# Optimization experiments

Measured on AMD Instinct MI355X. Metric: run time of the kernel, lower is better.

The kernel has to match this reference:

```python
import jax, jax.numpy as jnp
import numpy as np

B, C, H, W = 4, 512, 64, 64
CQ = C // 8  # query/key channels = 64


def setup_inputs() -> dict:
    key = jax.random.key(0)
    ks = jax.random.split(key, 6)
    return {
        "x_spatial": jax.random.normal(ks[0], (B, C, H, W), jnp.float32),
        "x_temporal": jax.random.normal(ks[1], (B, C, H, W), jnp.float32),
        "Wq": jax.random.normal(ks[2], (CQ, C), jnp.float32) * (1.0 / np.sqrt(C)),
        "bq": jnp.zeros((CQ,), jnp.float32),
        "Wk": jax.random.normal(ks[3], (CQ, C), jnp.float32) * (1.0 / np.sqrt(C)),
        "bk": jnp.zeros((CQ,), jnp.float32),
        "Wvs": jax.random.normal(ks[4], (C, C), jnp.float32) * (1.0 / np.sqrt(C)),
        "bvs": jnp.zeros((C,), jnp.float32),
        "Wvt": jax.random.normal(ks[5], (C, C), jnp.float32) * (1.0 / np.sqrt(C)),
        "bvt": jnp.zeros((C,), jnp.float32),
    }


def reference(x_spatial, x_temporal, Wq, bq, Wk, bk, Wvs, bvs, Wvt, bvt):
    b, c, h, w = x_spatial.shape
    n = h * w
    xs = x_spatial.reshape(b, c, n)   # (B, C, N)
    xt = x_temporal.reshape(b, c, n)
    # 1x1 convs == pointwise linear over channels
    q = jnp.einsum('qc,bcn->bnq', Wq, xs) + bq            # (B, N, CQ)
    k = jnp.einsum('qc,bcn->bqn', Wk, xt) + bk[:, None]    # (B, CQ, N)
    scale = (c // 8) ** -0.5
    energy = scale * jnp.einsum('bnq,bqm->bnm', q, k)      # (B, N, N)
    attn = jax.nn.softmax(energy, axis=-1)
    v_s = jnp.einsum('oc,bcn->bon', Wvs, xs) + bvs[:, None]  # (B, C, N)
    v_t = jnp.einsum('oc,bcn->bon', Wvt, xt) + bvt[:, None]
    # out[b,c,i] = sum_j v[b,c,j] * attn[b,i,j]
    out1 = jnp.einsum('bcj,bij->bci', v_s, attn)
    out2 = jnp.einsum('bcj,bij->bci', v_t, attn)
    out = out1.reshape(b, c, h, w) + x_spatial + out2.reshape(b, c, h, w) + x_temporal
    return out
```

## Files before the change

### kernel.cpp

```cpp
#include <hip/hip_runtime.h>
#include <hip/hip_bf16.h>
#include <math.h>

#define NTOK 4096
#define CH 512
#define CQD 64
#define NBATCH 4
#define JB 128

typedef __bf16 bf16x8 __attribute__((ext_vector_type(8)));
typedef float f32x4 __attribute__((ext_vector_type(4)));
typedef unsigned int u32x4 __attribute__((ext_vector_type(4)));
typedef unsigned short u16x4 __attribute__((ext_vector_type(4)));

__device__ __forceinline__ unsigned short f2bf(float f) {
  unsigned int u = __builtin_bit_cast(unsigned int, f);
  unsigned int r = (u + 0x7FFFu + ((u >> 16) & 1u)) >> 16;
  return (unsigned short)r;
}

__device__ __forceinline__ bf16x8 load_frag(const unsigned short* p) {
  u32x4 v = *reinterpret_cast<const u32x4*>(p);
  return __builtin_bit_cast(bf16x8, v);
}

__global__ void k_transpose(const float* __restrict__ xs, const float* __restrict__ xt,
                            unsigned short* __restrict__ xT) {
  __shared__ unsigned short lds[64][66];
  int b = blockIdx.z;
  int n0 = blockIdx.x * 64;
  int c0 = blockIdx.y * 64;
  const float* src = (c0 < CH) ? xs : xt;
  int cs0 = (c0 < CH) ? c0 : c0 - CH;
  int tid = threadIdx.x;
  int nn = tid & 63, cg = tid >> 6;
  const float* base = src + ((size_t)b * CH + cs0) * NTOK + n0;
  for (int cc = cg; cc < 64; cc += 4)
    lds[cc][nn] = f2bf(base[(size_t)cc * NTOK + nn]);
  __syncthreads();
  int cw = tid & 63, ng = tid >> 6;
  unsigned short* dst = xT + ((size_t)b * NTOK + n0) * 1024 + c0 + cw;
  for (int n2 = ng; n2 < 64; n2 += 4)
    dst[(size_t)n2 * 1024] = lds[cw][n2];
}

__global__ void k_weights(const float* __restrict__ Wq, const float* __restrict__ Wk,
                          const float* __restrict__ Wvs, const float* __restrict__ Wvt,
                          unsigned short* __restrict__ wq, unsigned short* __restrict__ wk,
                          unsigned short* __restrict__ wv) {
  int t = blockIdx.x * 256 + threadIdx.x;
  if (t < 32768) {
    wq[t] = f2bf(Wq[t]);
  } else if (t < 65536) {
    int j = t - 32768;
    wk[j] = f2bf(Wk[j]);
  } else {
    int j = t - 65536;
    if (j < 512 * 1024) {
      int c = j >> 10, k = j & 1023;
      float v = (k < 512) ? Wvs[c * 512 + k] : Wvt[c * 512 + (k - 512)];
      wv[j] = f2bf(v);
    }
  }
}

__global__ void __launch_bounds__(256)
k_proj(const unsigned short* __restrict__ xT, const unsigned short* __restrict__ W,
       const float* __restrict__ bias1, const float* __restrict__ bias2,
       unsigned short* __restrict__ out, int Kdim, int koff, int mode) {
  int b = blockIdx.z;
  int n0 = blockIdx.x * 256;
  int m0 = blockIdx.y * 64;
  int tid = threadIdx.x;
  int w = tid >> 6, l = tid & 63;
  int fr = l & 15, fk = l >> 4;
  f32x4 acc[4][4] = {};
  const unsigned short* xbase =
      xT + ((size_t)b * NTOK + n0 + w * 64 + fr) * 1024 + koff + fk * 8;
  const unsigned short* wbase = W + ((size_t)(m0 + fr)) * Kdim + fk * 8;
  for (int k = 0; k < Kdim; k += 32) {
    bf16x8 a[4], bb[4];
#pragma unroll
    for (int ns = 0; ns < 4; ns++) a[ns] = load_frag(xbase + (size_t)ns * 16 * 1024 + k);
#pragma unroll
    for (int mf = 0; mf < 4; mf++) bb[mf] = load_frag(wbase + (size_t)mf * 16 * Kdim + k);
#pragma unroll
    for (int ns = 0; ns < 4; ns++)
#pragma unroll
      for (int mf = 0; mf < 4; mf++)
        acc[ns][mf] = __builtin_amdgcn_mfma_f32_16x16x32_bf16(a[ns], bb[mf], acc[ns][mf], 0, 0, 0);
  }
  if (mode == 0) {
#pragma unroll
    for (int ns = 0; ns < 4; ns++)
#pragma unroll
      for (int mf = 0; mf < 4; mf++) {
        int m = m0 + mf * 16 + fr;
        float bv = bias1[m];
        int nb = n0 + w * 64 + ns * 16 + fk * 4;
#pragma unroll
        for (int r = 0; r < 4; r++)
          out[((size_t)b * NTOK + nb + r) * CQD + m] = f2bf(acc[ns][mf][r] + bv);
      }
  } else {
#pragma unroll
    for (int ns = 0; ns < 4; ns++)
#pragma unroll
      for (int mf = 0; mf < 4; mf++) {
        int c = m0 + mf * 16 + fr;
        float bv = bias1[c] + bias2[c];
        int nb = n0 + w * 64 + ns * 16 + fk * 4;
        u16x4 pk;
#pragma unroll
        for (int r = 0; r < 4; r++) pk[r] = f2bf(acc[ns][mf][r] + bv);
        *reinterpret_cast<u16x4*>(out + ((size_t)b * CH + c) * NTOK + nb) = pk;
      }
  }
}

__global__ void __launch_bounds__(512, 2)
k_pv(const unsigned short* __restrict__ Q, const unsigned short* __restrict__ Kt,
     const unsigned short* __restrict__ V, const float* __restrict__ xs,
     const float* __restrict__ xt, float* __restrict__ out) {
  __shared__ __align__(16) unsigned short P_lds[2][64 * JB];
  __shared__ float denom_lds[8][64];
  __shared__ float rden_lds[64];
  int b = blockIdx.y;
  int i0 = blockIdx.x * 64;
  int tid = threadIdx.x;
  int w = tid >> 6;
  int l = tid & 63;
  int fr = l & 15, fk = l >> 4;
  int c0 = w * 64;

  bf16x8 qf[4][2];
#pragma unroll
  for (int f = 0; f < 4; f++) {
    const unsigned short* qb = Q + ((size_t)b * NTOK + i0 + f * 16 + fr) * CQD + fk * 8;
    qf[f][0] = load_frag(qb);
    qf[f][1] = load_frag(qb + 32);
  }
  float dsum[4] = {0.f, 0.f, 0.f, 0.f};
  f32x4 acc[4][4] = {};

  const unsigned short* kbase = Kt + ((size_t)b * NTOK + w * 16 + fr) * CQD + fk * 8;
  const unsigned short* vbase = V + ((size_t)b * CH + c0 + fr) * NTOK + fk * 8;

  auto phaseA = [&](int jn, int buf) {
    bf16x8 kf0 = load_frag(kbase + (size_t)jn * CQD);
    bf16x8 kf1 = load_frag(kbase + (size_t)jn * CQD + 32);
    char* pb = reinterpret_cast<char*>(P_lds[buf]);
#pragma unroll
    for (int f = 0; f < 4; f++) {
      f32x4 s = {};
      s = __builtin_amdgcn_mfma_f32_16x16x32_bf16(kf0, qf[f][0], s, 0, 0, 0);
      s = __builtin_amdgcn_mfma_f32_16x16x32_bf16(kf1, qf[f][1], s, 0, 0, 0);
      u16x4 pk;
#pragma unroll
      for (int r = 0; r < 4; r++) {
        float p = __expf(0.125f * s[r] - 8.0f);
        dsum[f] += p;
        pk[r] = f2bf(p);
      }
      int prow = f * 16 + fr;
      int col = w * 32 + fk * 8;
      *reinterpret_cast<u16x4*>(pb + prow * (JB * 2) + (col ^ ((prow & 7) << 4))) = pk;
    }
  };

  phaseA(0, 0);
  __syncthreads();

  for (int t = 0; t < NTOK / JB; t++) {
    int cur = t & 1;
    int jc = t * JB;
    if (t < NTOK / JB - 1) phaseA(jc + JB, cur ^ 1);
    const char* pb = reinterpret_cast<const char*>(P_lds[cur]);
#pragma unroll
    for (int js = 0; js < 4; js++) {
      bf16x8 pa[4];
#pragma unroll
      for (int is = 0; is < 4; is++) {
        int prow = is * 16 + fr;
        int byteoff = prow * (JB * 2) + ((js * 64 + fk * 16) ^ ((prow & 7) << 4));
        pa[is] = __builtin_bit_cast(bf16x8,
                                    *reinterpret_cast<const u32x4*>(pb + byteoff));
      }
#pragma unroll
      for (int cf = 0; cf < 4; cf++) {
        bf16x8 vf = load_frag(vbase + (size_t)cf * 16 * NTOK + jc + js * 32);
#pragma unroll
        for (int is = 0; is < 4; is++)
          acc[is][cf] = __builtin_amdgcn_mfma_f32_16x16x32_bf16(pa[is], vf, acc[is][cf], 0, 0, 0);
      }
    }
    __syncthreads();
  }

#pragma unroll
  for (int f = 0; f < 4; f++) {
    float v = dsum[f];
    v += __shfl_xor(v, 16);
    v += __shfl_xor(v, 32);
    if (l < 16) denom_lds[w][f * 16 + l] = v;
  }
  __syncthreads();
  if (tid < 64) {
    float d = 0.f;
#pragma unroll
    for (int ww = 0; ww < 8; ww++) d += denom_lds[ww][tid];
    rden_lds[tid] = 1.0f / d;
  }
  __syncthreads();

#pragma unroll
  for (int is = 0; is < 4; is++)
#pragma unroll
    for (int cf = 0; cf < 4; cf++) {
      int c = c0 + cf * 16 + fr;
      size_t base = ((size_t)b * CH + c) * NTOK + i0 + is * 16 + fk * 4;
      f32x4 r1 = *reinterpret_cast<const f32x4*>(xs + base);
      f32x4 r2 = *reinterpret_cast<const f32x4*>(xt + base);
      f32x4 o;
#pragma unroll
      for (int r = 0; r < 4; r++)
        o[r] = acc[is][cf][r] * rden_lds[is * 16 + fk * 4 + r] + r1[r] + r2[r];
      *reinterpret_cast<f32x4*>(out + base) = o;
    }
}

extern "C" void kernel_launch(void* const* d_in, const int* in_sizes, int n_in,
                              void* d_out, int out_size, void* d_ws, size_t ws_size,
                              hipStream_t stream) {
  const float* xs  = (const float*)d_in[0];
  const float* xt  = (const float*)d_in[1];
  const float* Wq  = (const float*)d_in[2];
  const float* bq  = (const float*)d_in[3];
  const float* Wk  = (const float*)d_in[4];
  const float* bk  = (const float*)d_in[5];
  const float* Wvs = (const float*)d_in[6];
  const float* bvs = (const float*)d_in[7];
  const float* Wvt = (const float*)d_in[8];
  const float* bvt = (const float*)d_in[9];
  float* out = (float*)d_out;

  char* ws = (char*)d_ws;
  size_t off = 0;
  unsigned short* xT = (unsigned short*)(ws + off); off += (size_t)NBATCH * NTOK * 1024 * 2;
  unsigned short* wq = (unsigned short*)(ws + off); off += (size_t)64 * 512 * 2;
  unsigned short* wk = (unsigned short*)(ws + off); off += (size_t)64 * 512 * 2;
  unsigned short* wv = (unsigned short*)(ws + off); off += (size_t)512 * 1024 * 2;
  unsigned short* Qb  = (unsigned short*)(ws + off); off += (size_t)NBATCH * NTOK * CQD * 2;
  unsigned short* Ktb = (unsigned short*)(ws + off); off += (size_t)NBATCH * NTOK * CQD * 2;
  unsigned short* Vb  = (unsigned short*)(ws + off); off += (size_t)NBATCH * CH * NTOK * 2;
  if (ws_size < off) return;

  k_transpose<<<dim3(NTOK / 64, 16, NBATCH), 256, 0, stream>>>(xs, xt, xT);
  k_weights<<<dim3(2304), 256, 0, stream>>>(Wq, Wk, Wvs, Wvt, wq, wk, wv);
  k_proj<<<dim3(NTOK / 256, 1, NBATCH), 256, 0, stream>>>(xT, wq, bq, nullptr, Qb, 512, 0, 0);
  k_proj<<<dim3(NTOK / 256, 1, NBATCH), 256, 0, stream>>>(xT, wk, bk, nullptr, Ktb, 512, 512, 0);
  k_proj<<<dim3(NTOK / 256, 8, NBATCH), 256, 0, stream>>>(xT, wv, bvs, bvt, Vb, 1024, 0, 1);
  k_pv<<<dim3(NTOK / 64, NBATCH), 512, 0, stream>>>(Qb, Ktb, Vb, xs, xt, out);
}
```

Before: 297.4 us.

## Prefetch V and K fragments into registers and double-buffer P explicitly

Restructures the k_pv main loop into a two-stage software pipeline unrolled by two, with separate P0/P1 LDS buffers. All 16 V fragments for the next j-tile are loaded into registers ahead of the MFMA phase, and K fragments are loaded one tile early. This aims to hide global-load latency behind the matrix math. It also raises wave priority during the PV MFMA phase with s_setprio. The extra 64 VGPRs for the V prefetch, under launch_bounds(512,2), raise register pressure and risk spills or lower occupancy.

Result: faster. 285.7 us (-3.9%).

```diff
diff --git a/kernel.cpp b/kernel.cpp
--- a/kernel.cpp
+++ b/kernel.cpp
@@ -122,7 +122,8 @@
 k_pv(const unsigned short* __restrict__ Q, const unsigned short* __restrict__ Kt,
      const unsigned short* __restrict__ V, const float* __restrict__ xs,
      const float* __restrict__ xt, float* __restrict__ out) {
-  __shared__ __align__(16) unsigned short P_lds[2][64 * JB];
+  __shared__ __align__(16) unsigned short P0_lds[64 * JB];
+  __shared__ __align__(16) unsigned short P1_lds[64 * JB];
   __shared__ float denom_lds[8][64];
   __shared__ float rden_lds[64];
   int b = blockIdx.y;
@@ -146,10 +147,22 @@
   const unsigned short* kbase = Kt + ((size_t)b * NTOK + w * 16 + fr) * CQD + fk * 8;
   const unsigned short* vbase = V + ((size_t)b * CH + c0 + fr) * NTOK + fk * 8;
 
-  auto phaseA = [&](int jn, int buf) {
-    bf16x8 kf0 = load_frag(kbase + (size_t)jn * CQD);
-    bf16x8 kf1 = load_frag(kbase + (size_t)jn * CQD + 32);
-    char* pb = reinterpret_cast<char*>(P_lds[buf]);
+  bf16x8 kf0, kf1;
+  bf16x8 vf[16];
+
+  auto loadK = [&](int jn) {
+    kf0 = load_frag(kbase + (size_t)jn * CQD);
+    kf1 = load_frag(kbase + (size_t)jn * CQD + 32);
+  };
+  auto loadV = [&](int jc) {
+#pragma unroll
+    for (int cf = 0; cf < 4; cf++)
+#pragma unroll
+      for (int js = 0; js < 4; js++)
+        vf[cf * 4 + js] = load_frag(vbase + (size_t)cf * 16 * NTOK + jc + js * 32);
+  };
+  auto phaseA = [&](int jn, unsigned short* plds) {
+    char* pb = reinterpret_cast<char*>(plds);
 #pragma unroll
     for (int f = 0; f < 4; f++) {
       f32x4 s = {};
@@ -167,15 +180,9 @@
       *reinterpret_cast<u16x4*>(pb + prow * (JB * 2) + (col ^ ((prow & 7) << 4))) = pk;
     }
   };
-
-  phaseA(0, 0);
-  __syncthreads();
-
-  for (int t = 0; t < NTOK / JB; t++) {
-    int cur = t & 1;
-    int jc = t * JB;
-    if (t < NTOK / JB - 1) phaseA(jc + JB, cur ^ 1);
-    const char* pb = reinterpret_cast<const char*>(P_lds[cur]);
+  auto phaseB = [&](const unsigned short* plds) {
+    const char* pb = reinterpret_cast<const char*>(plds);
+    __builtin_amdgcn_s_setprio(1);
 #pragma unroll
     for (int js = 0; js < 4; js++) {
       bf16x8 pa[4];
@@ -183,18 +190,39 @@
       for (int is = 0; is < 4; is++) {
         int prow = is * 16 + fr;
         int byteoff = prow * (JB * 2) + ((js * 64 + fk * 16) ^ ((prow & 7) << 4));
-        pa[is] = __builtin_bit_cast(bf16x8,
-                                    *reinterpret_cast<const u32x4*>(pb + byteoff));
+        pa[is] = __builtin_bit_cast(bf16x8, *reinterpret_cast<const u32x4*>(pb + byteoff));
       }
 #pragma unroll
       for (int cf = 0; cf < 4; cf++) {
-        bf16x8 vf = load_frag(vbase + (size_t)cf * 16 * NTOK + jc + js * 32);
 #pragma unroll
         for (int is = 0; is < 4; is++)
-          acc[is][cf] = __builtin_amdgcn_mfma_f32_16x16x32_bf16(pa[is], vf, acc[is][cf], 0, 0, 0);
-      }
-    }
+          acc[is][cf] =
+              __builtin_amdgcn_mfma_f32_16x16x32_bf16(pa[is], vf[cf * 4 + js], acc[is][cf], 0, 0, 0);
+      }
+    }
+    __builtin_amdgcn_s_setprio(0);
+  };
+
+  constexpr int NT = NTOK / JB;
+  loadK(0);
+  loadV(0);
+  phaseA(0, P0_lds);
+  loadK(JB);
+  __syncthreads();
+
+  for (int t = 0; t < NT; t += 2) {
+    phaseA((t + 1) * JB, P1_lds);
+    if (t + 2 < NT) loadK((t + 2) * JB);
+    phaseB(P0_lds);
     __syncthreads();
+    loadV((t + 1) * JB);
+    if (t + 2 < NT) {
+      phaseA((t + 2) * JB, P0_lds);
+      if (t + 3 < NT) loadK((t + 3) * JB);
+    }
+    phaseB(P1_lds);
+    __syncthreads();
+    if (t + 2 < NT) loadV((t + 2) * JB);
   }
 
 #pragma unroll
```
